# Kernel tuning notes

Hardware: AMD Instinct MI355X
Metric: run time of the kernel (lower is better)

Reference implementation:

```python
import jax, jax.numpy as jnp
import numpy as np

B, D, H, E = 1024, 2048, 2048, 16
K = 8            # args.topk
ENERGY_T = 1.0   # args.energy_T
EXP_ID = 0       # args.id (anchor expert)
DROP = 0.2       # hard-coded dropout_coefficient
KEEP = int(K * (1.0 - DROP))  # 6


def setup_inputs() -> dict:
    key = jax.random.key(0)
    ks = jax.random.split(key, 5)
    x = jax.random.normal(ks[0], (B, D), dtype=jnp.float32)
    Wg = jax.random.normal(ks[1], (D, E), dtype=jnp.float32) * 0.02
    bg = jnp.zeros((E,), dtype=jnp.float32)
    We = jax.random.normal(ks[2], (E, D, H), dtype=jnp.float32) * 0.02
    be = jnp.zeros((E, H), dtype=jnp.float32)
    return {"x": x, "Wg": Wg, "bg": bg, "We": We, "be": be}


def reference(x, Wg, bg, We, be):
    # gating: softmax over experts, then top-k (sorted descending, as torch.topk)
    gate = jax.nn.softmax(x @ Wg + bg, axis=-1)          # [B, E]
    vals, idx = jax.lax.top_k(gate, K)                   # [B, K]

    # all expert outputs (E is small; cheaper than gathering [B,K,D,H] weights)
    out_all = jnp.einsum('bd,edh->beh', x, We) + be      # [B, E, H]
    out_k = jnp.take_along_axis(out_all, idx[:, :, None], axis=1)  # [B, K, H]

    # elementwise cosine similarity vs. anchor expert output
    rep = out_all[:, EXP_ID]                             # [B, H]
    cos = (rep[:, None, :] * out_k) / (
        jnp.abs(rep)[:, None, :] * jnp.abs(out_k) + 1e-8)
    cos = jnp.where((idx == EXP_ID)[:, :, None], 1.0, cos)

    # energy/confidence H_k = T * logsumexp(cos / T) over feature dim
    energy = ENERGY_T * jax.nn.logsumexp(cos / ENERGY_T, axis=-1)  # [B, K]

    # keep the KEEP lowest-energy experts (stable sort, as python list.sort)
    keep_pos = jnp.argsort(energy, axis=-1)[:, :KEEP]    # [B, KEEP]
    vals_kept = jnp.take_along_axis(vals, keep_pos, axis=1)           # [B, KEEP]
    out_kept = jnp.take_along_axis(out_k, keep_pos[:, :, None], axis=1)  # [B, KEEP, H]

    return jnp.sum(vals_kept[:, :, None] * out_kept, axis=1)  # [B, H]
```

## Files before the change

### kernel.cpp

```cpp
#include <hip/hip_runtime.h>
#include <math.h>

#define B_ 1024
#define D_ 2048
#define H_ 2048
#define E_ 16
#define K_ 8
#define KEEP_ 6
#define EXP_ID_ 0

#define WS_OUTALL 0
#define WS_IDX    134217728
#define WS_VALS   (134217728 + 32768)
#define WS_ENERGY (134217728 + 65536)
#define WS_CNT    (134217728 + 98304)
#define WS_ROWS   (134217728 + 98560)

__global__ void init_cnt_kernel(int* __restrict__ cnt) {
  if (threadIdx.x < E_) cnt[threadIdx.x] = 0;
}

__global__ __launch_bounds__(64) void gate_kernel(
    const float* __restrict__ x, const float* __restrict__ Wg,
    const float* __restrict__ bg, int* __restrict__ idx, float* __restrict__ vals,
    int* __restrict__ cnt, int* __restrict__ rows) {
  const int b = blockIdx.x;
  const int lane = threadIdx.x;
  double acc[E_];
#pragma unroll
  for (int e = 0; e < E_; ++e) acc[e] = 0.0;
  for (int d = lane; d < D_; d += 64) {
    double xv = (double)x[(size_t)b * D_ + d];
    const float* w = Wg + (size_t)d * E_;
#pragma unroll
    for (int e = 0; e < E_; ++e) acc[e] = fma(xv, (double)w[e], acc[e]);
  }
  for (int off = 32; off > 0; off >>= 1) {
#pragma unroll
    for (int e = 0; e < E_; ++e) acc[e] += __shfl_down(acc[e], off, 64);
  }
  if (lane == 0) {
    double logit[E_];
#pragma unroll
    for (int e = 0; e < E_; ++e) logit[e] = acc[e] + (double)bg[e];
    double m = logit[0];
#pragma unroll
    for (int e = 1; e < E_; ++e) m = fmax(m, logit[e]);
    double p[E_], s = 0.0;
#pragma unroll
    for (int e = 0; e < E_; ++e) { p[e] = exp(logit[e] - m); s += p[e]; }
#pragma unroll
    for (int e = 0; e < E_; ++e) p[e] = p[e] / s;
    unsigned taken = 0;
    for (int j = 0; j < K_; ++j) {
      int best = -1; double bv = -1.0;
#pragma unroll
      for (int e = 0; e < E_; ++e)
        if (!((taken >> e) & 1u) && p[e] > bv) { bv = p[e]; best = e; }
      taken |= (1u << best);
      idx[b * K_ + j] = best;
      vals[b * K_ + j] = (float)bv;
    }
    taken |= 1u;
#pragma unroll
    for (int e = 0; e < E_; ++e) {
      if ((taken >> e) & 1u) {
        int p2 = atomicAdd(&cnt[e], 1);
        rows[e * B_ + p2] = b;
      }
    }
  }
}

#define BM 64
#define BN 64
#define BK 16

__global__ __launch_bounds__(256) void gemm_expert_kernel(
    const float* __restrict__ X, const float* __restrict__ We,
    const float* __restrict__ be, float* __restrict__ out_all,
    const int* __restrict__ cnt, const int* __restrict__ rows) {
  const int e  = blockIdx.z;
  const int nrows = cnt[e];
  const int m0 = blockIdx.y * BM;
  if (m0 >= nrows) return;
  const int n0 = blockIdx.x * BN;
  const float* Bmat = We + (size_t)e * D_ * H_;
  const int* rl = rows + e * B_;

  __shared__ double As[BM][BK + 2];
  __shared__ double Bs[BK][BN + 2];

  const int tid = threadIdx.x;
  const int tx = tid % 16, ty = tid / 16;
  const int arow  = tid >> 2;
  const int acol4 = (tid & 3) * 4;
  const int brow  = tid >> 4;
  const int bcol4 = (tid & 15) * 4;

  const int gidx = m0 + arow;
  const int grow = rl[(gidx < nrows) ? gidx : (nrows - 1)];
  const float* aptr = X + (size_t)grow * D_;
  const float* bptr = Bmat + (size_t)brow * H_ + n0 + bcol4;

  const int c0 = tx * 2;
  const int c1 = tx * 2 + 32;

  double acc[4][4] = {};

  float4 av = *(const float4*)(aptr + acol4);
  float4 bv = *(const float4*)(bptr);

  for (int k0 = 0; k0 < D_; k0 += BK) {
    __syncthreads();
    *(double2*)&As[arow][acol4 + 0] = make_double2((double)av.x, (double)av.y);
    *(double2*)&As[arow][acol4 + 2] = make_double2((double)av.z, (double)av.w);
    *(double2*)&Bs[brow][bcol4 + 0] = make_double2((double)bv.x, (double)bv.y);
    *(double2*)&Bs[brow][bcol4 + 2] = make_double2((double)bv.z, (double)bv.w);
    __syncthreads();
    if (k0 + BK < D_) {
      av = *(const float4*)(aptr + (k0 + BK) + acol4);
      bv = *(const float4*)(bptr + (size_t)(k0 + BK) * H_);
    }
#pragma unroll
    for (int kk = 0; kk < BK; kk += 2) {
      double2 a0p = *(const double2*)&As[ty * 4 + 0][kk];
      double2 a1p = *(const double2*)&As[ty * 4 + 1][kk];
      double2 a2p = *(const double2*)&As[ty * 4 + 2][kk];
      double2 a3p = *(const double2*)&As[ty * 4 + 3][kk];
      double2 b01a = *(const double2*)&Bs[kk][c0];
      double2 b23a = *(const double2*)&Bs[kk][c1];
      double2 b01b = *(const double2*)&Bs[kk + 1][c0];
      double2 b23b = *(const double2*)&Bs[kk + 1][c1];
      acc[0][0] = fma(a0p.x, b01a.x, acc[0][0]);
      acc[0][1] = fma(a0p.x, b01a.y, acc[0][1]);
      acc[0][2] = fma(a0p.x, b23a.x, acc[0][2]);
      acc[0][3] = fma(a0p.x, b23a.y, acc[0][3]);
      acc[1][0] = fma(a1p.x, b01a.x, acc[1][0]);
      acc[1][1] = fma(a1p.x, b01a.y, acc[1][1]);
      acc[1][2] = fma(a1p.x, b23a.x, acc[1][2]);
      acc[1][3] = fma(a1p.x, b23a.y, acc[1][3]);
      acc[2][0] = fma(a2p.x, b01a.x, acc[2][0]);
      acc[2][1] = fma(a2p.x, b01a.y, acc[2][1]);
      acc[2][2] = fma(a2p.x, b23a.x, acc[2][2]);
      acc[2][3] = fma(a2p.x, b23a.y, acc[2][3]);
      acc[3][0] = fma(a3p.x, b01a.x, acc[3][0]);
      acc[3][1] = fma(a3p.x, b01a.y, acc[3][1]);
      acc[3][2] = fma(a3p.x, b23a.x, acc[3][2]);
      acc[3][3] = fma(a3p.x, b23a.y, acc[3][3]);
      acc[0][0] = fma(a0p.y, b01b.x, acc[0][0]);
      acc[0][1] = fma(a0p.y, b01b.y, acc[0][1]);
      acc[0][2] = fma(a0p.y, b23b.x, acc[0][2]);
      acc[0][3] = fma(a0p.y, b23b.y, acc[0][3]);
      acc[1][0] = fma(a1p.y, b01b.x, acc[1][0]);
      acc[1][1] = fma(a1p.y, b01b.y, acc[1][1]);
      acc[1][2] = fma(a1p.y, b23b.x, acc[1][2]);
      acc[1][3] = fma(a1p.y, b23b.y, acc[1][3]);
      acc[2][0] = fma(a2p.y, b01b.x, acc[2][0]);
      acc[2][1] = fma(a2p.y, b01b.y, acc[2][1]);
      acc[2][2] = fma(a2p.y, b23b.x, acc[2][2]);
      acc[2][3] = fma(a2p.y, b23b.y, acc[2][3]);
      acc[3][0] = fma(a3p.y, b01b.x, acc[3][0]);
      acc[3][1] = fma(a3p.y, b01b.y, acc[3][1]);
      acc[3][2] = fma(a3p.y, b23b.x, acc[3][2]);
      acc[3][3] = fma(a3p.y, b23b.y, acc[3][3]);
    }
  }
#pragma unroll
  for (int i = 0; i < 4; ++i) {
    const int ridx = m0 + ty * 4 + i;
    if (ridx < nrows) {
      const int m = rl[ridx];
      float* dst = out_all + ((size_t)m * E_ + e) * H_ + n0;
      float2 p0, p1;
      p0.x = (float)(acc[i][0] + (double)be[(size_t)e * H_ + n0 + c0 + 0]);
      p0.y = (float)(acc[i][1] + (double)be[(size_t)e * H_ + n0 + c0 + 1]);
      p1.x = (float)(acc[i][2] + (double)be[(size_t)e * H_ + n0 + c1 + 0]);
      p1.y = (float)(acc[i][3] + (double)be[(size_t)e * H_ + n0 + c1 + 1]);
      *(float2*)(dst + c0) = p0;
      *(float2*)(dst + c1) = p1;
    }
  }
}

__global__ __launch_bounds__(256) void energy_kernel(
    const float* __restrict__ out_all, const int* __restrict__ idx,
    float* __restrict__ energy) {
  const int b = blockIdx.x, j = blockIdx.y, t = threadIdx.x;
  const int e = idx[b * K_ + j];
  if (e == EXP_ID_) {
    if (t == 0) energy[b * K_ + j] = 1.0f + (float)log(2048.0);
    return;
  }
  const float* rep = out_all + ((size_t)b * E_ + EXP_ID_) * H_;
  const float* ok  = out_all + ((size_t)b * E_ + e) * H_;

  __shared__ float cs[H_];
  __shared__ float red[256];
  __shared__ float chain[128];

  float mx = -2.0f;
  for (int h = t; h < H_; h += 256) {
    float r = rep[h], o = ok[h];
    float num = r * o;
    float den = fabsf(r) * fabsf(o) + 1e-8f;
    float c = num / den;
    cs[h] = c;
    mx = fmaxf(mx, c);
  }
  red[t] = mx;
  __syncthreads();
  for (int off = 128; off > 0; off >>= 1) {
    if (t < off) red[t] = fmaxf(red[t], red[t + off]);
    __syncthreads();
  }
  const float m = red[0];
  __syncthreads();

  if (t < 128) {
    const int blk = t >> 3, jj = t & 7;
    const float* base = cs + blk * 128;
    float d0 = base[jj] - m;
    float r = (float)exp((double)d0);
#pragma unroll
    for (int q = 1; q < 16; ++q) {
      float dq = base[q * 8 + jj] - m;
      float term = (float)exp((double)dq);
      r = r + term;
    }
    chain[t] = r;
  }
  __syncthreads();

  if (t == 0) {
    float Bsum[16];
#pragma unroll
    for (int blk = 0; blk < 16; ++blk) {
      const float* c8 = chain + blk * 8;
      float s01 = c8[0] + c8[1];
      float s23 = c8[2] + c8[3];
      float s45 = c8[4] + c8[5];
      float s67 = c8[6] + c8[7];
      Bsum[blk] = (s01 + s23) + (s45 + s67);
    }
    float C[8], D[4], Ee[2];
#pragma unroll
    for (int i = 0; i < 8; ++i) C[i] = Bsum[2 * i] + Bsum[2 * i + 1];
#pragma unroll
    for (int i = 0; i < 4; ++i) D[i] = C[2 * i] + C[2 * i + 1];
#pragma unroll
    for (int i = 0; i < 2; ++i) Ee[i] = D[2 * i] + D[2 * i + 1];
    float S = Ee[0] + Ee[1];
    energy[b * K_ + j] = m + (float)log((double)S);
  }
}

__global__ __launch_bounds__(256) void final_kernel(
    const float* __restrict__ out_all, const int* __restrict__ idx,
    const float* __restrict__ vals, const float* __restrict__ energy,
    float* __restrict__ out) {
  const int b = blockIdx.x;
  const int h = blockIdx.y * 256 + threadIdx.x;
  float En[K_];
#pragma unroll
  for (int j = 0; j < K_; ++j) En[j] = energy[b * K_ + j];
  double s = 0.0;
#pragma unroll
  for (int j = 0; j < K_; ++j) {
    int pos = 0;
#pragma unroll
    for (int j2 = 0; j2 < K_; ++j2)
      pos += (En[j2] < En[j]) || (En[j2] == En[j] && j2 < j);
    if (pos < KEEP_) {
      int e = idx[b * K_ + j];
      s += (double)vals[b * K_ + j] *
           (double)out_all[((size_t)b * E_ + e) * H_ + h];
    }
  }
  out[(size_t)b * H_ + h] = (float)s;
}

extern "C" void kernel_launch(void* const* d_in, const int* in_sizes, int n_in,
                              void* d_out, int out_size, void* d_ws, size_t ws_size,
                              hipStream_t stream) {
  const float* x  = (const float*)d_in[0];
  const float* Wg = (const float*)d_in[1];
  const float* bg = (const float*)d_in[2];
  const float* We = (const float*)d_in[3];
  const float* be = (const float*)d_in[4];
  float* out = (float*)d_out;

  char* ws = (char*)d_ws;
  float* out_all = (float*)(ws + WS_OUTALL);
  int*   idx     = (int*)(ws + WS_IDX);
  float* vals    = (float*)(ws + WS_VALS);
  float* energy  = (float*)(ws + WS_ENERGY);
  int*   cnt     = (int*)(ws + WS_CNT);
  int*   rows    = (int*)(ws + WS_ROWS);

  init_cnt_kernel<<<dim3(1), dim3(64), 0, stream>>>(cnt);

  gate_kernel<<<dim3(B_), dim3(64), 0, stream>>>(x, Wg, bg, idx, vals, cnt, rows);

  gemm_expert_kernel<<<dim3(H_ / BN, B_ / BM, E_), dim3(256), 0, stream>>>(
      x, We, be, out_all, cnt, rows);

  energy_kernel<<<dim3(B_, K_), dim3(256), 0, stream>>>(out_all, idx, energy);

  final_kernel<<<dim3(B_, H_ / 256), dim3(256), 0, stream>>>(
      out_all, idx, vals, energy, out);
}
```

Measured before the change: 1.778 ms.

## Use FP64 MFMA for expert GEMM with runtime-probed output layout

Adds an FP64 MFMA path (16x16x4 f64) to the expert GEMM, replacing the scalar double FMA inner loop with matrix-core instructions. A tiny probe kernel runs the MFMA once per call to discover the accumulator row/column mapping and checks correctness, setting a flag. The GEMM reads that flag and falls back to the old path if the probe fails. The cost is an extra launch, plus table lookups in the epilogue and stores that are not coalesced.

```diff
diff --git a/kernel.cpp b/kernel.cpp
--- a/kernel.cpp
+++ b/kernel.cpp
@@ -9,15 +9,49 @@
 #define KEEP_ 6
 #define EXP_ID_ 0
 
+typedef double v4d __attribute__((ext_vector_type(4)));
+
 #define WS_OUTALL 0
 #define WS_IDX    134217728
 #define WS_VALS   (134217728 + 32768)
 #define WS_ENERGY (134217728 + 65536)
 #define WS_CNT    (134217728 + 98304)
 #define WS_ROWS   (134217728 + 98560)
-
-__global__ void init_cnt_kernel(int* __restrict__ cnt) {
+#define WS_ROWTAB (134217728 + 164096)
+#define WS_COLTAB (134217728 + 165120)
+#define WS_OKFLG  (134217728 + 166144)
+
+__global__ void init_cnt_kernel(int* __restrict__ cnt, int* __restrict__ okflg) {
   if (threadIdx.x < E_) cnt[threadIdx.x] = 0;
+  if (threadIdx.x == 0) okflg[0] = 1;
+}
+
+__global__ __launch_bounds__(64) void mfma_probe_kernel(
+    int* __restrict__ rowtab, int* __restrict__ coltab, int* __restrict__ okflg) {
+  const int l = threadIdx.x;
+  const v4d z = {0.0, 0.0, 0.0, 0.0};
+  double a1 = (double)(l & 15);
+  double b1 = ((l >> 4) == 0) ? 1.0 : 0.0;
+  v4d d1 = __builtin_amdgcn_mfma_f64_16x16x4f64(a1, b1, z, 0, 0, 0);
+  double a2 = ((l >> 4) == 0) ? 1.0 : 0.0;
+  double b2 = (double)(l & 15);
+  v4d d2 = __builtin_amdgcn_mfma_f64_16x16x4f64(a2, b2, z, 0, 0, 0);
+  double a3 = (double)((l & 15) + 1);
+  double b3 = (double)((l & 15) + 1);
+  v4d d3 = __builtin_amdgcn_mfma_f64_16x16x4f64(a3, b3, z, 0, 0, 0);
+
+  int ok = 1;
+#pragma unroll
+  for (int g = 0; g < 4; ++g) {
+    int r = (int)(d1[g] + 0.5);
+    int c = (int)(d2[g] + 0.5);
+    if (r < 0 || r > 15 || c < 0 || c > 15) { r = 0; c = 0; ok = 0; }
+    rowtab[l * 4 + g] = r;
+    coltab[l * 4 + g] = c;
+    double expect = 4.0 * (double)(r + 1) * (double)(c + 1);
+    if (d3[g] != expect) ok = 0;
+  }
+  if (!ok) okflg[0] = 0;
 }
 
 __global__ __launch_bounds__(64) void gate_kernel(
@@ -79,7 +113,9 @@
 __global__ __launch_bounds__(256) void gemm_expert_kernel(
     const float* __restrict__ X, const float* __restrict__ We,
     const float* __restrict__ be, float* __restrict__ out_all,
-    const int* __restrict__ cnt, const int* __restrict__ rows) {
+    const int* __restrict__ cnt, const int* __restrict__ rows,
+    const int* __restrict__ rowtab, const int* __restrict__ coltab,
+    const int* __restrict__ okflg) {
   const int e  = blockIdx.z;
   const int nrows = cnt[e];
   const int m0 = blockIdx.y * BM;
@@ -92,7 +128,6 @@
   __shared__ double Bs[BK][BN + 2];
 
   const int tid = threadIdx.x;
-  const int tx = tid % 16, ty = tid / 16;
   const int arow  = tid >> 2;
   const int acol4 = (tid & 3) * 4;
   const int brow  = tid >> 4;
@@ -103,6 +138,65 @@
   const float* aptr = X + (size_t)grow * D_;
   const float* bptr = Bmat + (size_t)brow * H_ + n0 + bcol4;
 
+  const bool use_mfma = (okflg[0] == 1);
+
+  if (use_mfma) {
+    const int lane = tid & 63;
+    const int wave = tid >> 6;
+    const int lr = lane & 15;
+    const int lq = lane >> 4;
+
+    v4d acc[4];
+#pragma unroll
+    for (int c = 0; c < 4; ++c) acc[c] = (v4d){0.0, 0.0, 0.0, 0.0};
+
+    float4 av = *(const float4*)(aptr + acol4);
+    float4 bv = *(const float4*)(bptr);
+
+    for (int k0 = 0; k0 < D_; k0 += BK) {
+      __syncthreads();
+      *(double2*)&As[arow][acol4 + 0] = make_double2((double)av.x, (double)av.y);
+      *(double2*)&As[arow][acol4 + 2] = make_double2((double)av.z, (double)av.w);
+      *(double2*)&Bs[brow][bcol4 + 0] = make_double2((double)bv.x, (double)bv.y);
+      *(double2*)&Bs[brow][bcol4 + 2] = make_double2((double)bv.z, (double)bv.w);
+      __syncthreads();
+      if (k0 + BK < D_) {
+        av = *(const float4*)(aptr + (k0 + BK) + acol4);
+        bv = *(const float4*)(bptr + (size_t)(k0 + BK) * H_);
+      }
+#pragma unroll
+      for (int k4 = 0; k4 < BK; k4 += 4) {
+        double a = As[wave * 16 + lr][k4 + lq];
+#pragma unroll
+        for (int c = 0; c < 4; ++c) {
+          double bb = Bs[k4 + lq][c * 16 + lr];
+          acc[c] = __builtin_amdgcn_mfma_f64_16x16x4f64(a, bb, acc[c], 0, 0, 0);
+        }
+      }
+    }
+    int drow[4], dcol[4];
+#pragma unroll
+    for (int g = 0; g < 4; ++g) {
+      drow[g] = rowtab[lane * 4 + g];
+      dcol[g] = coltab[lane * 4 + g];
+    }
+#pragma unroll
+    for (int c = 0; c < 4; ++c) {
+#pragma unroll
+      for (int g = 0; g < 4; ++g) {
+        const int ridx = m0 + wave * 16 + drow[g];
+        if (ridx < nrows) {
+          const int mrow = rl[ridx];
+          const int col = n0 + c * 16 + dcol[g];
+          out_all[((size_t)mrow * E_ + e) * H_ + col] =
+              (float)(acc[c][g] + (double)be[(size_t)e * H_ + col]);
+        }
+      }
+    }
+    return;
+  }
+
+  const int tx = tid % 16, ty = tid / 16;
   const int c0 = tx * 2;
   const int c1 = tx * 2 + 32;
 
@@ -297,13 +391,18 @@
   float* energy  = (float*)(ws + WS_ENERGY);
   int*   cnt     = (int*)(ws + WS_CNT);
   int*   rows    = (int*)(ws + WS_ROWS);
-
-  init_cnt_kernel<<<dim3(1), dim3(64), 0, stream>>>(cnt);
+  int*   rowtab  = (int*)(ws + WS_ROWTAB);
+  int*   coltab  = (int*)(ws + WS_COLTAB);
+  int*   okflg   = (int*)(ws + WS_OKFLG);
+
+  init_cnt_kernel<<<dim3(1), dim3(64), 0, stream>>>(cnt, okflg);
+
+  mfma_probe_kernel<<<dim3(1), dim3(64), 0, stream>>>(rowtab, coltab, okflg);
 
   gate_kernel<<<dim3(B_), dim3(64), 0, stream>>>(x, Wg, bg, idx, vals, cnt, rows);
 
   gemm_expert_kernel<<<dim3(H_ / BN, B_ / BM, E_), dim3(256), 0, stream>>>(
-      x, We, be, out_all, cnt, rows);
+      x, We, be, out_all, cnt, rows, rowtab, coltab, okflg);
 
   energy_kernel<<<dim3(B_, K_), dim3(256), 0, stream>>>(out_all, idx, energy);
 
```

Measured after the change: 1.677 ms. -5.6%, faster.
